# Kernel tuning notes

Measured on AMD Instinct MI355X. Metric: run time of the kernel, lower is better.

## Reference

```python
import jax, jax.numpy as jnp
import numpy as np
import math

N_NODES = 100000
N_EDGES = 3200000
NFEAT = 512
NHID = 256
NCLASS = 16
NLAYERS = 8
LAMDA = 0.5
ALPHA = 0.1


def setup_inputs() -> dict:
    key = jax.random.key(0)
    ks = jax.random.split(key, 10)
    x = jax.random.normal(ks[0], (N_NODES, NFEAT), dtype=jnp.float32)
    edge_src = jax.random.randint(ks[1], (N_EDGES,), 0, N_NODES, dtype=jnp.int32)
    edge_dst = jax.random.randint(ks[2], (N_EDGES,), 0, N_NODES, dtype=jnp.int32)
    edge_w = jax.random.uniform(ks[3], (N_EDGES,), dtype=jnp.float32)
    # fcs[0]: Linear(nfeat, nhidden); fcs[1]: Linear(nhidden, nclass)
    s0 = 1.0 / math.sqrt(NFEAT)
    w0 = jax.random.uniform(ks[4], (NFEAT, NHID), minval=-s0, maxval=s0, dtype=jnp.float32)
    b0 = jax.random.uniform(ks[5], (NHID,), minval=-s0, maxval=s0, dtype=jnp.float32)
    # conv weights: uniform(-1/sqrt(out_features), +), out_features = nhidden
    sc = 1.0 / math.sqrt(NHID)
    conv_w = jax.random.uniform(ks[6], (NLAYERS, NHID, NHID), minval=-sc, maxval=sc, dtype=jnp.float32)
    w1 = jax.random.uniform(ks[7], (NHID, NCLASS), minval=-sc, maxval=sc, dtype=jnp.float32)
    b1 = jax.random.uniform(ks[8], (NCLASS,), minval=-sc, maxval=sc, dtype=jnp.float32)
    return {"x": x, "edge_src": edge_src, "edge_dst": edge_dst, "edge_w": edge_w,
            "w0": w0, "b0": b0, "conv_w": conv_w, "w1": w1, "b1": b1}


def _spmm(edge_src, edge_dst, edge_w, h):
    # torch.spmm(adj, h): out[i] = sum_j adj[i,j] * h[j], adj in COO (dst=row, src=col)
    msgs = edge_w[:, None] * h[edge_src]            # [E, H] irregular gather
    return jax.ops.segment_sum(msgs, edge_dst, num_segments=h.shape[0])


def reference(x, edge_src, edge_dst, edge_w, w0, b0, conv_w, w1, b1):
    # eval mode: F.dropout is identity
    h = jax.nn.relu(x @ w0 + b0)                    # [N, NHID]
    h0 = h
    for i in range(NLAYERS):
        theta = math.log(LAMDA / (i + 1) + 1.0)
        hi = _spmm(edge_src, edge_dst, edge_w, h)   # sparse aggregate
        support = (1.0 - ALPHA) * hi + ALPHA * h0   # initial residual (GCNII)
        out = theta * (support @ conv_w[i]) + (1.0 - theta) * support
        h = jax.nn.relu(out + h)                    # layer residual
    return jax.nn.sigmoid(h @ w1 + b1)              # [N, NCLASS]
```

## Files before the change

### kernel.cpp

```cpp
#include <hip/hip_runtime.h>
#include <math.h>

#define N_NODES 100000
#define N_EDGES 3200000
#define NFEAT 512
#define NHID 256
#define NCLASS 16
#define NLAYERS 8

#define SCAN_CHUNK 1024
#define NB ((N_NODES + SCAN_CHUNK - 1) / SCAN_CHUNK)

typedef float f32x4 __attribute__((ext_vector_type(4)));
typedef short s16x8 __attribute__((ext_vector_type(8)));

__device__ __forceinline__ unsigned short bf16_rne(float f) {
  unsigned u = __float_as_uint(f);
  unsigned r = 0x7fffu + ((u >> 16) & 1u);
  return (unsigned short)((u + r) >> 16);
}
__device__ __forceinline__ float bf16_tof(unsigned short h) {
  return __uint_as_float(((unsigned)h) << 16);
}

__device__ __forceinline__ void async16(void* lds_dst, const void* gsrc) {
  __builtin_amdgcn_global_load_lds(
      (const __attribute__((address_space(1))) unsigned int*)gsrc,
      (__attribute__((address_space(3))) unsigned int*)lds_dst, 16, 0, 0);
}

__global__ void k_hist(const int* __restrict__ dst, int* __restrict__ cnt) {
  int i = blockIdx.x * 256 + threadIdx.x;
  if (i < N_EDGES) atomicAdd(&cnt[dst[i]], 1);
}

__global__ void k_blocksum(const int* __restrict__ cnt, int* __restrict__ bs) {
  __shared__ int red[256];
  int b = blockIdx.x, t = threadIdx.x;
  int s = 0;
  int base = b * SCAN_CHUNK;
  for (int j = 0; j < 4; ++j) {
    int i = base + t + j * 256;
    if (i < N_NODES) s += cnt[i];
  }
  red[t] = s;
  __syncthreads();
  for (int off = 128; off > 0; off >>= 1) {
    if (t < off) red[t] += red[t + off];
    __syncthreads();
  }
  if (t == 0) bs[b] = red[0];
}

__global__ void k_scan_top(int* __restrict__ bs, int* __restrict__ rp) {
  if (threadIdx.x == 0) {
    int run = 0;
    for (int b = 0; b < NB; ++b) { int v = bs[b]; bs[b] = run; run += v; }
    rp[N_NODES] = run;
  }
}

__global__ void k_scan_write(const int* __restrict__ cnt, const int* __restrict__ bs,
                             int* __restrict__ rp) {
  __shared__ int tot[256];
  int b = blockIdx.x, t = threadIdx.x;
  int base = b * SCAN_CHUNK + t * 4;
  int v0 = 0, v1 = 0, v2 = 0, v3 = 0;
  if (base + 0 < N_NODES) v0 = cnt[base + 0];
  if (base + 1 < N_NODES) v1 = cnt[base + 1];
  if (base + 2 < N_NODES) v2 = cnt[base + 2];
  if (base + 3 < N_NODES) v3 = cnt[base + 3];
  int tsum = v0 + v1 + v2 + v3;
  tot[t] = tsum;
  __syncthreads();
  for (int off = 1; off < 256; off <<= 1) {
    int v = 0;
    if (t >= off) v = tot[t - off];
    __syncthreads();
    if (t >= off) tot[t] += v;
    __syncthreads();
  }
  int excl = tot[t] - tsum + bs[b];
  if (base + 0 < N_NODES) rp[base + 0] = excl;
  if (base + 1 < N_NODES) rp[base + 1] = excl + v0;
  if (base + 2 < N_NODES) rp[base + 2] = excl + v0 + v1;
  if (base + 3 < N_NODES) rp[base + 3] = excl + v0 + v1 + v2;
}

__global__ void k_fill(const int* __restrict__ src, const int* __restrict__ dst,
                       const float* __restrict__ w, const int* __restrict__ rp,
                       int* __restrict__ fill, int* __restrict__ col,
                       float* __restrict__ val) {
  int i = blockIdx.x * 256 + threadIdx.x;
  if (i < N_EDGES) {
    int d = dst[i];
    int pos = rp[d] + atomicAdd(&fill[d], 1);
    col[pos] = src[i];
    val[pos] = w[i];
  }
}

__global__ __launch_bounds__(256)
void k_spmm_half(const int* __restrict__ rp, const int* __restrict__ col,
                 const float* __restrict__ val, const float* __restrict__ h,
                 const float* __restrict__ h0,
                 unsigned short* __restrict__ sup_hi,
                 unsigned short* __restrict__ sup_lo, int f0) {
  int wave = threadIdx.x >> 6;
  int lane = threadIdx.x & 63;
  int node = blockIdx.x * 4 + wave;
  if (node >= N_NODES) return;
  int e0 = rp[node], e1 = rp[node + 1];
  const float2* __restrict__ hv = (const float2*)h;
  int fo = (f0 >> 1) + lane;

  float2 a0 = make_float2(0.f, 0.f);
  float2 a1 = make_float2(0.f, 0.f);
  float2 a2 = make_float2(0.f, 0.f);
  float2 a3 = make_float2(0.f, 0.f);

  int e = e0;
  for (; e + 4 <= e1; e += 4) {
    int s0 = col[e], s1 = col[e + 1], s2 = col[e + 2], s3 = col[e + 3];
    float w0 = val[e], w1 = val[e + 1], w2 = val[e + 2], w3 = val[e + 3];
    float2 v0 = hv[(size_t)s0 * 128 + fo];
    float2 v1 = hv[(size_t)s1 * 128 + fo];
    float2 v2 = hv[(size_t)s2 * 128 + fo];
    float2 v3 = hv[(size_t)s3 * 128 + fo];
    a0.x += w0 * v0.x; a0.y += w0 * v0.y;
    a1.x += w1 * v1.x; a1.y += w1 * v1.y;
    a2.x += w2 * v2.x; a2.y += w2 * v2.y;
    a3.x += w3 * v3.x; a3.y += w3 * v3.y;
  }
  for (; e < e1; ++e) {
    int s0 = col[e];
    float w0 = val[e];
    float2 v0 = hv[(size_t)s0 * 128 + fo];
    a0.x += w0 * v0.x; a0.y += w0 * v0.y;
  }

  float2 acc;
  acc.x = (a0.x + a1.x) + (a2.x + a3.x);
  acc.y = (a0.y + a1.y) + (a2.y + a3.y);

  float2 z = ((const float2*)h0)[(size_t)node * 128 + fo];
  float ox = 0.9f * acc.x + 0.1f * z.x;
  float oy = 0.9f * acc.y + 0.1f * z.y;
  unsigned short hx = bf16_rne(ox), hy = bf16_rne(oy);
  unsigned short lx = bf16_rne(ox - bf16_tof(hx));
  unsigned short ly = bf16_rne(oy - bf16_tof(hy));
  ((ushort2*)sup_hi)[(size_t)node * 128 + fo] = make_ushort2(hx, hy);
  ((ushort2*)sup_lo)[(size_t)node * 128 + fo] = make_ushort2(lx, ly);
}

__global__ void k_splitw(const float* __restrict__ W, unsigned short* __restrict__ hi,
                         unsigned short* __restrict__ lo, int K) {
  int mat = blockIdx.y;
  const float* Wm = W + (size_t)mat * K * NHID;
  unsigned short* hm = hi + (size_t)mat * K * NHID;
  unsigned short* lm = lo + (size_t)mat * K * NHID;
  int idx = blockIdx.x * 256 + threadIdx.x;
  if (idx >= K * NHID) return;
  int k = idx >> 8;
  int n = idx & 255;
  float f = Wm[idx];
  unsigned short h = bf16_rne(f);
  unsigned short l = bf16_rne(f - bf16_tof(h));
  hm[(size_t)n * K + k] = h;
  lm[(size_t)n * K + k] = l;
}

template <int MODE>
__global__ __launch_bounds__(512)
void k_gemm2(const float* __restrict__ Af,
             const unsigned short* __restrict__ Ah_g,
             const unsigned short* __restrict__ Al_g,
             const unsigned short* __restrict__ Bh_g,
             const unsigned short* __restrict__ Bl_g, int K,
             const float* __restrict__ bias, const float* __restrict__ hin,
             float* __restrict__ out1, float* __restrict__ out2, float theta) {
  __shared__ unsigned short pool[49152];
  const int tid = threadIdx.x;
  const int lane = tid & 63, w = tid >> 6;
  const int wr = w >> 2, wc = w & 3;
  const int l16 = lane & 15, lk = lane >> 4;
  const int bm = blockIdx.x * 128;

  f32x4 acc[4][4];
#pragma unroll
  for (int i = 0; i < 4; ++i)
#pragma unroll
    for (int j = 0; j < 4; ++j)
#pragma unroll
      for (int q = 0; q < 4; ++q) acc[i][j][q] = 0.f;

  auto stageB = [&](int buf, int kc) {
#pragma unroll
    for (int u = 0; u < 2; ++u) {
      int fb = w * 2 + u;
      size_t go = (size_t)(fb * 16 + l16) * K + kc + lk * 8;
      async16(&pool[16384 + buf * 8192 + fb * 512], &Bh_g[go]);
      async16(&pool[32768 + buf * 8192 + fb * 512], &Bl_g[go]);
    }
  };
  auto stageA1 = [&](int buf, int kc) {
    size_t go = (size_t)(bm + w * 16 + l16) * K + kc + lk * 8;
    async16(&pool[0 + buf * 4096 + w * 512], &Ah_g[go]);
    async16(&pool[8192 + buf * 4096 + w * 512], &Al_g[go]);
  };
  float4 fa0, fa1;
  auto stageA0_issue = [&](int kc) {
    int m0 = tid >> 3, k00 = (tid & 7) * 4;
    int m1 = (tid + 512) >> 3, k01 = ((tid + 512) & 7) * 4;
    fa0 = make_float4(0.f, 0.f, 0.f, 0.f);
    fa1 = fa0;
    if (bm + m0 < N_NODES) fa0 = *(const float4*)&Af[(size_t)(bm + m0) * K + kc + k00];
    if (bm + m1 < N_NODES) fa1 = *(const float4*)&Af[(size_t)(bm + m1) * K + kc + k01];
  };
  auto stageA0_write = [&](int buf) {
#pragma unroll
    for (int p = 0; p < 2; ++p) {
      int f = tid + p * 512;
      int m = f >> 3, k0 = (f & 7) * 4;
      float4 fv = p ? fa1 : fa0;
      int L = (m >> 4) * 64 + (m & 15) + (k0 >> 3) * 16;
      unsigned short h0 = bf16_rne(fv.x), h1 = bf16_rne(fv.y);
      unsigned short h2 = bf16_rne(fv.z), h3 = bf16_rne(fv.w);
      ushort4 hv = make_ushort4(h0, h1, h2, h3);
      ushort4 lv = make_ushort4(bf16_rne(fv.x - bf16_tof(h0)),
                                bf16_rne(fv.y - bf16_tof(h1)),
                                bf16_rne(fv.z - bf16_tof(h2)),
                                bf16_rne(fv.w - bf16_tof(h3)));
      *(ushort4*)&pool[0 + buf * 4096 + L * 8 + (k0 & 7)] = hv;
      *(ushort4*)&pool[8192 + buf * 4096 + L * 8 + (k0 & 7)] = lv;
    }
  };

  if (MODE == 0) { stageA0_issue(0); stageA0_write(0); }
  else stageA1(0, 0);
  stageB(0, 0);
  __syncthreads();

  const int nt = K / 32;
  int buf = 0;
  for (int t = 0; t < nt; ++t) {
    const bool pf = (t + 1 < nt);
    if (pf) {
      if (MODE == 0) stageA0_issue((t + 1) * 32);
      else stageA1(buf ^ 1, (t + 1) * 32);
      stageB(buf ^ 1, (t + 1) * 32);
    }
    s16x8 ah[4], al[4], bh[4], bl[4];
#pragma unroll
    for (int i = 0; i < 4; ++i) {
      int fb = wr * 4 + i;
      ah[i] = *(const s16x8*)&pool[0 + buf * 4096 + fb * 512 + lane * 8];
      al[i] = *(const s16x8*)&pool[8192 + buf * 4096 + fb * 512 + lane * 8];
    }
#pragma unroll
    for (int j = 0; j < 4; ++j) {
      int fb = wc * 4 + j;
      bh[j] = *(const s16x8*)&pool[16384 + buf * 8192 + fb * 512 + lane * 8];
      bl[j] = *(const s16x8*)&pool[32768 + buf * 8192 + fb * 512 + lane * 8];
    }
#pragma unroll
    for (int i = 0; i < 4; ++i)
#pragma unroll
      for (int j = 0; j < 4; ++j)
        acc[i][j] = __builtin_amdgcn_mfma_f32_16x16x32_bf16(ah[i], bh[j], acc[i][j], 0, 0, 0);
#pragma unroll
    for (int i = 0; i < 4; ++i)
#pragma unroll
      for (int j = 0; j < 4; ++j)
        acc[i][j] = __builtin_amdgcn_mfma_f32_16x16x32_bf16(ah[i], bl[j], acc[i][j], 0, 0, 0);
#pragma unroll
    for (int i = 0; i < 4; ++i)
#pragma unroll
      for (int j = 0; j < 4; ++j)
        acc[i][j] = __builtin_amdgcn_mfma_f32_16x16x32_bf16(al[i], bh[j], acc[i][j], 0, 0, 0);
    if (MODE == 0 && pf) stageA0_write(buf ^ 1);
    __syncthreads();
    buf ^= 1;
  }

  float* Cst = (float*)pool;
  const float omt = 1.f - theta;
  for (int g = 0; g < 4; ++g) {
    if (wr == (g >> 1)) {
#pragma unroll
      for (int ii = 0; ii < 2; ++ii) {
        int i = (g & 1) * 2 + ii;
#pragma unroll
        for (int j = 0; j < 4; ++j) {
          int colc = wc * 64 + j * 16 + l16;
#pragma unroll
          for (int q = 0; q < 4; ++q) {
            int lr = ii * 16 + lk * 4 + q;
            Cst[lr * 260 + colc] = acc[i][j][q];
          }
        }
      }
    }
    __syncthreads();
#pragma unroll
    for (int p = 0; p < 4; ++p) {
      int f = tid + p * 512;
      int row = f >> 6, c4 = (f & 63) * 4;
      int gm = bm + g * 32 + row;
      if (gm < N_NODES) {
        float4 v = *(const float4*)&Cst[row * 260 + c4];
        size_t r = (size_t)gm * NHID + c4;
        float4 o;
        if (MODE == 0) {
          float4 bb = *(const float4*)&bias[c4];
          o.x = fmaxf(v.x + bb.x, 0.f);
          o.y = fmaxf(v.y + bb.y, 0.f);
          o.z = fmaxf(v.z + bb.z, 0.f);
          o.w = fmaxf(v.w + bb.w, 0.f);
          *(float4*)&out1[r] = o;
          *(float4*)&out2[r] = o;
        } else {
          ushort4 sh = *(const ushort4*)&Ah_g[r];
          ushort4 sl = *(const ushort4*)&Al_g[r];
          float4 hv = *(const float4*)&hin[r];
          float sx = bf16_tof(sh.x) + bf16_tof(sl.x);
          float sy = bf16_tof(sh.y) + bf16_tof(sl.y);
          float sz = bf16_tof(sh.z) + bf16_tof(sl.z);
          float sw = bf16_tof(sh.w) + bf16_tof(sl.w);
          o.x = fmaxf(theta * v.x + omt * sx + hv.x, 0.f);
          o.y = fmaxf(theta * v.y + omt * sy + hv.y, 0.f);
          o.z = fmaxf(theta * v.z + omt * sz + hv.z, 0.f);
          o.w = fmaxf(theta * v.w + omt * sw + hv.w, 0.f);
          *(float4*)&out1[r] = o;
        }
      }
    }
    __syncthreads();
  }
}

__global__ __launch_bounds__(256)
void k_final(const float* __restrict__ h, const float* __restrict__ w1,
             const float* __restrict__ b1, float* __restrict__ out) {
  __shared__ float ws[NHID * NCLASS];
  int t = threadIdx.x;
  for (int i = t; i < NHID * NCLASS; i += 256) ws[i] = w1[i];
  __syncthreads();
  int node = blockIdx.x * 16 + (t >> 4);
  int c = t & 15;
  if (node >= N_NODES) return;
  float acc = b1[c];
  const float* hr = &h[(size_t)node * NHID];
  for (int k = 0; k < NHID; k += 4) {
    float4 hv = *(const float4*)&hr[k];
    acc += hv.x * ws[(k + 0) * NCLASS + c];
    acc += hv.y * ws[(k + 1) * NCLASS + c];
    acc += hv.z * ws[(k + 2) * NCLASS + c];
    acc += hv.w * ws[(k + 3) * NCLASS + c];
  }
  out[(size_t)node * NCLASS + c] = 1.f / (1.f + __expf(-acc));
}

extern "C" void kernel_launch(void* const* d_in, const int* in_sizes, int n_in,
                              void* d_out, int out_size, void* d_ws, size_t ws_size,
                              hipStream_t stream) {
  const float* x        = (const float*)d_in[0];
  const int*   edge_src = (const int*)d_in[1];
  const int*   edge_dst = (const int*)d_in[2];
  const float* edge_w   = (const float*)d_in[3];
  const float* w0       = (const float*)d_in[4];
  const float* b0       = (const float*)d_in[5];
  const float* conv_w   = (const float*)d_in[6];
  const float* w1       = (const float*)d_in[7];
  const float* b1       = (const float*)d_in[8];
  float* out = (float*)d_out;

  char* ws = (char*)d_ws;
  size_t off = 0;
  auto alloc = [&](size_t bytes) {
    size_t o = off;
    off = (off + bytes + 255) & ~(size_t)255;
    return (void*)(ws + o);
  };
  float* h    = (float*)alloc((size_t)N_NODES * NHID * 4);
  float* h0   = (float*)alloc((size_t)N_NODES * NHID * 4);
  unsigned short* sup_hi = (unsigned short*)alloc((size_t)N_NODES * NHID * 2);
  unsigned short* sup_lo = (unsigned short*)alloc((size_t)N_NODES * NHID * 2);
  int*   col = (int*)alloc((size_t)N_EDGES * 4);
  float* val = (float*)alloc((size_t)N_EDGES * 4);
  int*   rp  = (int*)alloc((size_t)(N_NODES + 1) * 4);
  int*   cnt = (int*)alloc((size_t)N_NODES * 4);
  int*   bs  = (int*)alloc((size_t)NB * 4);
  unsigned short* w0t_hi = (unsigned short*)alloc((size_t)NFEAT * NHID * 2);
  unsigned short* w0t_lo = (unsigned short*)alloc((size_t)NFEAT * NHID * 2);
  unsigned short* cwt_hi = (unsigned short*)alloc((size_t)NLAYERS * NHID * NHID * 2);
  unsigned short* cwt_lo = (unsigned short*)alloc((size_t)NLAYERS * NHID * NHID * 2);
  (void)ws_size;

  (void)hipMemsetAsync(cnt, 0, (size_t)N_NODES * 4, stream);
  k_hist<<<(N_EDGES + 255) / 256, 256, 0, stream>>>(edge_dst, cnt);
  k_blocksum<<<NB, 256, 0, stream>>>(cnt, bs);
  k_scan_top<<<1, 64, 0, stream>>>(bs, rp);
  k_scan_write<<<NB, 256, 0, stream>>>(cnt, bs, rp);
  (void)hipMemsetAsync(cnt, 0, (size_t)N_NODES * 4, stream);
  k_fill<<<(N_EDGES + 255) / 256, 256, 0, stream>>>(edge_src, edge_dst, edge_w, rp,
                                                    cnt, col, val);

  k_splitw<<<dim3((NFEAT * NHID + 255) / 256, 1), 256, 0, stream>>>(w0, w0t_hi, w0t_lo, NFEAT);
  k_splitw<<<dim3((NHID * NHID + 255) / 256, NLAYERS), 256, 0, stream>>>(conv_w, cwt_hi, cwt_lo, NHID);

  int gblocks = (N_NODES + 127) / 128;
  k_gemm2<0><<<gblocks, 512, 0, stream>>>(x, nullptr, nullptr, w0t_hi, w0t_lo,
                                          NFEAT, b0, nullptr, h, h0, 0.f);

  for (int i = 0; i < NLAYERS; ++i) {
    float theta = logf(0.5f / (float)(i + 1) + 1.0f);
    k_spmm_half<<<(N_NODES + 3) / 4, 256, 0, stream>>>(rp, col, val, h, h0,
                                                       sup_hi, sup_lo, 0);
    k_spmm_half<<<(N_NODES + 3) / 4, 256, 0, stream>>>(rp, col, val, h, h0,
                                                       sup_hi, sup_lo, 128);
    const unsigned short* whi = cwt_hi + (size_t)i * NHID * NHID;
    const unsigned short* wlo = cwt_lo + (size_t)i * NHID * NHID;
    k_gemm2<1><<<gblocks, 512, 0, stream>>>(nullptr, sup_hi, sup_lo, whi, wlo,
                                            NHID, nullptr, h, h, nullptr, theta);
  }

  k_final<<<(N_NODES + 15) / 16, 256, 0, stream>>>(h, w1, b1, out);
}
```

Measured before the change: 5.297 ms.

## Interleave CSR col/val and split SpMM into feature quarters on even layers

Stores edge column and weight together as int2 so each edge needs one 8-byte load instead of two separate loads. Unrolls the SpMM gather loop to 8 independent accumulators to keep more loads in flight. Adds a 64-feature-slice SpMM kernel used on even layers, which shrinks the gathered working set per pass so more of it can stay in cache. The cost is four passes over the edge list instead of two. Odd layers keep the two-pass half kernel, which effectively compares the two strategies.

```diff
diff --git a/kernel.cpp b/kernel.cpp
--- a/kernel.cpp
+++ b/kernel.cpp
@@ -89,23 +89,20 @@
 
 __global__ void k_fill(const int* __restrict__ src, const int* __restrict__ dst,
                        const float* __restrict__ w, const int* __restrict__ rp,
-                       int* __restrict__ fill, int* __restrict__ col,
-                       float* __restrict__ val) {
+                       int* __restrict__ fill, int2* __restrict__ cv) {
   int i = blockIdx.x * 256 + threadIdx.x;
   if (i < N_EDGES) {
     int d = dst[i];
     int pos = rp[d] + atomicAdd(&fill[d], 1);
-    col[pos] = src[i];
-    val[pos] = w[i];
+    cv[pos] = make_int2(src[i], __float_as_int(w[i]));
   }
 }
 
 __global__ __launch_bounds__(256)
-void k_spmm_half(const int* __restrict__ rp, const int* __restrict__ col,
-                 const float* __restrict__ val, const float* __restrict__ h,
-                 const float* __restrict__ h0,
-                 unsigned short* __restrict__ sup_hi,
-                 unsigned short* __restrict__ sup_lo, int f0) {
+void k_spmm_h(const int* __restrict__ rp, const int2* __restrict__ cv,
+              const float* __restrict__ h, const float* __restrict__ h0,
+              unsigned short* __restrict__ sup_hi,
+              unsigned short* __restrict__ sup_lo, int f0) {
   int wave = threadIdx.x >> 6;
   int lane = threadIdx.x & 63;
   int node = blockIdx.x * 4 + wave;
@@ -114,34 +111,44 @@
   const float2* __restrict__ hv = (const float2*)h;
   int fo = (f0 >> 1) + lane;
 
-  float2 a0 = make_float2(0.f, 0.f);
-  float2 a1 = make_float2(0.f, 0.f);
-  float2 a2 = make_float2(0.f, 0.f);
-  float2 a3 = make_float2(0.f, 0.f);
+  float2 a0 = make_float2(0.f, 0.f), a1 = a0, a2 = a0, a3 = a0;
+  float2 a4 = a0, a5 = a0, a6 = a0, a7 = a0;
 
   int e = e0;
-  for (; e + 4 <= e1; e += 4) {
-    int s0 = col[e], s1 = col[e + 1], s2 = col[e + 2], s3 = col[e + 3];
-    float w0 = val[e], w1 = val[e + 1], w2 = val[e + 2], w3 = val[e + 3];
-    float2 v0 = hv[(size_t)s0 * 128 + fo];
-    float2 v1 = hv[(size_t)s1 * 128 + fo];
-    float2 v2 = hv[(size_t)s2 * 128 + fo];
-    float2 v3 = hv[(size_t)s3 * 128 + fo];
+  for (; e + 8 <= e1; e += 8) {
+    int2 c0 = cv[e + 0], c1 = cv[e + 1], c2 = cv[e + 2], c3 = cv[e + 3];
+    int2 c4 = cv[e + 4], c5 = cv[e + 5], c6 = cv[e + 6], c7 = cv[e + 7];
+    float2 v0 = hv[(size_t)c0.x * 128 + fo];
+    float2 v1 = hv[(size_t)c1.x * 128 + fo];
+    float2 v2 = hv[(size_t)c2.x * 128 + fo];
+    float2 v3 = hv[(size_t)c3.x * 128 + fo];
+    float2 v4 = hv[(size_t)c4.x * 128 + fo];
+    float2 v5 = hv[(size_t)c5.x * 128 + fo];
+    float2 v6 = hv[(size_t)c6.x * 128 + fo];
+    float2 v7 = hv[(size_t)c7.x * 128 + fo];
+    float w0 = __int_as_float(c0.y), w1 = __int_as_float(c1.y);
+    float w2 = __int_as_float(c2.y), w3 = __int_as_float(c3.y);
+    float w4 = __int_as_float(c4.y), w5 = __int_as_float(c5.y);
+    float w6 = __int_as_float(c6.y), w7 = __int_as_float(c7.y);
     a0.x += w0 * v0.x; a0.y += w0 * v0.y;
     a1.x += w1 * v1.x; a1.y += w1 * v1.y;
     a2.x += w2 * v2.x; a2.y += w2 * v2.y;
     a3.x += w3 * v3.x; a3.y += w3 * v3.y;
+    a4.x += w4 * v4.x; a4.y += w4 * v4.y;
+    a5.x += w5 * v5.x; a5.y += w5 * v5.y;
+    a6.x += w6 * v6.x; a6.y += w6 * v6.y;
+    a7.x += w7 * v7.x; a7.y += w7 * v7.y;
   }
   for (; e < e1; ++e) {
-    int s0 = col[e];
-    float w0 = val[e];
-    float2 v0 = hv[(size_t)s0 * 128 + fo];
-    a0.x += w0 * v0.x; a0.y += w0 * v0.y;
+    int2 c = cv[e];
+    float w = __int_as_float(c.y);
+    float2 v = hv[(size_t)c.x * 128 + fo];
+    a0.x += w * v.x; a0.y += w * v.y;
   }
 
   float2 acc;
-  acc.x = (a0.x + a1.x) + (a2.x + a3.x);
-  acc.y = (a0.y + a1.y) + (a2.y + a3.y);
+  acc.x = ((a0.x + a1.x) + (a2.x + a3.x)) + ((a4.x + a5.x) + (a6.x + a7.x));
+  acc.y = ((a0.y + a1.y) + (a2.y + a3.y)) + ((a4.y + a5.y) + (a6.y + a7.y));
 
   float2 z = ((const float2*)h0)[(size_t)node * 128 + fo];
   float ox = 0.9f * acc.x + 0.1f * z.x;
@@ -151,6 +158,56 @@
   unsigned short ly = bf16_rne(oy - bf16_tof(hy));
   ((ushort2*)sup_hi)[(size_t)node * 128 + fo] = make_ushort2(hx, hy);
   ((ushort2*)sup_lo)[(size_t)node * 128 + fo] = make_ushort2(lx, ly);
+}
+
+__global__ __launch_bounds__(256)
+void k_spmm_q(const int* __restrict__ rp, const int2* __restrict__ cv,
+              const float* __restrict__ h, const float* __restrict__ h0,
+              unsigned short* __restrict__ sup_hi,
+              unsigned short* __restrict__ sup_lo, int f0) {
+  int wave = threadIdx.x >> 6;
+  int lane = threadIdx.x & 63;
+  int node = blockIdx.x * 4 + wave;
+  if (node >= N_NODES) return;
+  int e0 = rp[node], e1 = rp[node + 1];
+  int fo = f0 + lane;
+
+  float a0 = 0.f, a1 = 0.f, a2 = 0.f, a3 = 0.f;
+  float a4 = 0.f, a5 = 0.f, a6 = 0.f, a7 = 0.f;
+
+  int e = e0;
+  for (; e + 8 <= e1; e += 8) {
+    int2 c0 = cv[e + 0], c1 = cv[e + 1], c2 = cv[e + 2], c3 = cv[e + 3];
+    int2 c4 = cv[e + 4], c5 = cv[e + 5], c6 = cv[e + 6], c7 = cv[e + 7];
+    float v0 = h[(size_t)c0.x * 256 + fo];
+    float v1 = h[(size_t)c1.x * 256 + fo];
+    float v2 = h[(size_t)c2.x * 256 + fo];
+    float v3 = h[(size_t)c3.x * 256 + fo];
+    float v4 = h[(size_t)c4.x * 256 + fo];
+    float v5 = h[(size_t)c5.x * 256 + fo];
+    float v6 = h[(size_t)c6.x * 256 + fo];
+    float v7 = h[(size_t)c7.x * 256 + fo];
+    a0 += __int_as_float(c0.y) * v0;
+    a1 += __int_as_float(c1.y) * v1;
+    a2 += __int_as_float(c2.y) * v2;
+    a3 += __int_as_float(c3.y) * v3;
+    a4 += __int_as_float(c4.y) * v4;
+    a5 += __int_as_float(c5.y) * v5;
+    a6 += __int_as_float(c6.y) * v6;
+    a7 += __int_as_float(c7.y) * v7;
+  }
+  for (; e < e1; ++e) {
+    int2 c = cv[e];
+    a0 += __int_as_float(c.y) * h[(size_t)c.x * 256 + fo];
+  }
+
+  float acc = ((a0 + a1) + (a2 + a3)) + ((a4 + a5) + (a6 + a7));
+  float z = h0[(size_t)node * 256 + fo];
+  float o = 0.9f * acc + 0.1f * z;
+  unsigned short hh = bf16_rne(o);
+  unsigned short ll = bf16_rne(o - bf16_tof(hh));
+  sup_hi[(size_t)node * 256 + fo] = hh;
+  sup_lo[(size_t)node * 256 + fo] = ll;
 }
 
 __global__ void k_splitw(const float* __restrict__ W, unsigned short* __restrict__ hi,
@@ -386,8 +443,7 @@
   float* h0   = (float*)alloc((size_t)N_NODES * NHID * 4);
   unsigned short* sup_hi = (unsigned short*)alloc((size_t)N_NODES * NHID * 2);
   unsigned short* sup_lo = (unsigned short*)alloc((size_t)N_NODES * NHID * 2);
-  int*   col = (int*)alloc((size_t)N_EDGES * 4);
-  float* val = (float*)alloc((size_t)N_EDGES * 4);
+  int2*  cv  = (int2*)alloc((size_t)N_EDGES * 8);
   int*   rp  = (int*)alloc((size_t)(N_NODES + 1) * 4);
   int*   cnt = (int*)alloc((size_t)N_NODES * 4);
   int*   bs  = (int*)alloc((size_t)NB * 4);
@@ -404,7 +460,7 @@
   k_scan_write<<<NB, 256, 0, stream>>>(cnt, bs, rp);
   (void)hipMemsetAsync(cnt, 0, (size_t)N_NODES * 4, stream);
   k_fill<<<(N_EDGES + 255) / 256, 256, 0, stream>>>(edge_src, edge_dst, edge_w, rp,
-                                                    cnt, col, val);
+                                                    cnt, cv);
 
   k_splitw<<<dim3((NFEAT * NHID + 255) / 256, 1), 256, 0, stream>>>(w0, w0t_hi, w0t_lo, NFEAT);
   k_splitw<<<dim3((NHID * NHID + 255) / 256, NLAYERS), 256, 0, stream>>>(conv_w, cwt_hi, cwt_lo, NHID);
@@ -415,10 +471,15 @@
 
   for (int i = 0; i < NLAYERS; ++i) {
     float theta = logf(0.5f / (float)(i + 1) + 1.0f);
-    k_spmm_half<<<(N_NODES + 3) / 4, 256, 0, stream>>>(rp, col, val, h, h0,
-                                                       sup_hi, sup_lo, 0);
-    k_spmm_half<<<(N_NODES + 3) / 4, 256, 0, stream>>>(rp, col, val, h, h0,
-                                                       sup_hi, sup_lo, 128);
+    if ((i & 1) == 0) {
+      for (int f0 = 0; f0 < NHID; f0 += 64)
+        k_spmm_q<<<(N_NODES + 3) / 4, 256, 0, stream>>>(rp, cv, h, h0,
+                                                        sup_hi, sup_lo, f0);
+    } else {
+      for (int f0 = 0; f0 < NHID; f0 += 128)
+        k_spmm_h<<<(N_NODES + 3) / 4, 256, 0, stream>>>(rp, cv, h, h0,
+                                                        sup_hi, sup_lo, f0);
+    }
     const unsigned short* whi = cwt_hi + (size_t)i * NHID * NHID;
     const unsigned short* wlo = cwt_lo + (size_t)i * NHID * NHID;
     k_gemm2<1><<<gblocks, 512, 0, stream>>>(nullptr, sup_hi, sup_lo, whi, wlo,
```

New measurement: 5.440 ms. 2.7% more time.
